# Kernel tuning notes

Hardware: AMD Instinct MI355X
Metric: run time of the kernel (lower is better)

Reference implementation:

```python
import jax, jax.numpy as jnp
import numpy as np

EMBED_DIM = 768
NUM_HEADS = 12
HEAD_DIM = EMBED_DIM // NUM_HEADS
MLP_RATIO = 4.0
HIDDEN_DIM = int(EMBED_DIM * MLP_RATIO)
B, N = 8, 1024


def setup_inputs() -> dict:
    key = jax.random.key(0)
    ks = jax.random.split(key, 12)
    d = EMBED_DIM
    h = HIDDEN_DIM
    s = lambda fan_in: 1.0 / np.sqrt(fan_in)
    return {
        "x": jax.random.normal(ks[0], (B, N, d), dtype=jnp.float32),
        "ln1_w": jnp.ones((d,), jnp.float32),
        "ln1_b": jnp.zeros((d,), jnp.float32),
        "qkv_w": jax.random.normal(ks[1], (3 * d, d), jnp.float32) * s(d),
        "qkv_b": jnp.zeros((3 * d,), jnp.float32),
        "proj_w": jax.random.normal(ks[2], (d, d), jnp.float32) * s(d),
        "proj_b": jnp.zeros((d,), jnp.float32),
        "ln2_w": jnp.ones((d,), jnp.float32),
        "ln2_b": jnp.zeros((d,), jnp.float32),
        "fc1_w": jax.random.normal(ks[3], (h, d), jnp.float32) * s(d),
        "fc1_b": jnp.zeros((h,), jnp.float32),
        "fc2_w": jax.random.normal(ks[4], (d, h), jnp.float32) * s(h),
        "fc2_b": jnp.zeros((d,), jnp.float32),
    }


def _layernorm(x, w, b, eps=1e-5):
    mu = jnp.mean(x, axis=-1, keepdims=True)
    var = jnp.var(x, axis=-1, keepdims=True)
    return (x - mu) * jax.lax.rsqrt(var + eps) * w + b


def _attention(x, qkv_w, qkv_b, proj_w, proj_b):
    b, n, c = x.shape
    qkv = x @ qkv_w.T + qkv_b  # [B, N, 3C]
    qkv = qkv.reshape(b, n, 3, NUM_HEADS, HEAD_DIM)
    q, k, v = jnp.moveaxis(qkv, 2, 0)  # each [B, N, H, Dh]
    scale = HEAD_DIM ** -0.5
    attn = jnp.einsum("bqhd,bkhd->bhqk", q, k) * scale  # [B, H, N, N]
    attn = jax.nn.softmax(attn, axis=-1)
    out = jnp.einsum("bhqk,bkhd->bqhd", attn, v).reshape(b, n, c)
    return out @ proj_w.T + proj_b


def reference(x, ln1_w, ln1_b, qkv_w, qkv_b, proj_w, proj_b,
              ln2_w, ln2_b, fc1_w, fc1_b, fc2_w, fc2_b):
    x = x + _attention(_layernorm(x, ln1_w, ln1_b), qkv_w, qkv_b, proj_w, proj_b)
    h = _layernorm(x, ln2_w, ln2_b)
    h = jax.nn.gelu(h @ fc1_w.T + fc1_b, approximate=False)
    x = x + (h @ fc2_w.T + fc2_b)
    return x
```

## Files before the change

### kernel.cpp

```cpp
#include <hip/hip_runtime.h>
#include <hip/hip_bf16.h>
#include <math.h>

typedef __attribute__((ext_vector_type(8))) short bf16x8;
typedef __attribute__((ext_vector_type(4))) float f32x4;
typedef unsigned short ushort_t;

#define GLOAD(srcp, dstp) __builtin_amdgcn_global_load_lds((const __attribute__((address_space(1))) void*)(srcp), (__attribute__((address_space(3))) void*)(dstp), 16, 0, 0)

__device__ inline ushort_t f2bfn(float f){
  union{ __bf16 h; ushort_t u; } c;
  c.h = (__bf16)f;
  return c.u;
}

__global__ __launch_bounds__(256) void cvt_all(const float* __restrict__ q, const float* __restrict__ p,
                                               const float* __restrict__ f1, const float* __restrict__ f2w,
                                               ushort_t* __restrict__ dq, ushort_t* __restrict__ dp,
                                               ushort_t* __restrict__ d1, ushort_t* __restrict__ d2){
  int i4 = blockIdx.x*256 + threadIdx.x;
  const float* src; ushort_t* dst; int off;
  if(i4 < 442368){ src=q;  dst=dq; off=i4; }
  else if(i4 < 589824){ src=p;  dst=dp; off=i4-442368; }
  else if(i4 < 1179648){ src=f1; dst=d1; off=i4-589824; }
  else { src=f2w; dst=d2; off=i4-1179648; }
  int i = off*4;
  float4 v = *(const float4*)(src+i);
  ushort4 o; o.x=f2bfn(v.x); o.y=f2bfn(v.y); o.z=f2bfn(v.z); o.w=f2bfn(v.w);
  *(ushort4*)(dst+i) = o;
}

__global__ __launch_bounds__(192) void ln_kernel(const float* __restrict__ x, const float* __restrict__ w,
                                                 const float* __restrict__ b, ushort_t* __restrict__ out){
  int row = blockIdx.x, t = threadIdx.x;
  const float4 v = *(const float4*)(x + (size_t)row*768 + t*4);
  float s  = v.x+v.y+v.z+v.w;
  float s2 = v.x*v.x+v.y*v.y+v.z*v.z+v.w*v.w;
  for(int m=1;m<64;m<<=1){ s += __shfl_xor(s,m,64); s2 += __shfl_xor(s2,m,64); }
  __shared__ float ls[3], ls2[3];
  int wv_ = t>>6;
  if((t&63)==0){ ls[wv_]=s; ls2[wv_]=s2; }
  __syncthreads();
  s = ls[0]+ls[1]+ls[2]; s2 = ls2[0]+ls2[1]+ls2[2];
  float mu = s*(1.f/768.f);
  float var = s2*(1.f/768.f) - mu*mu;
  float rs = rsqrtf(var + 1e-5f);
  float4 wv4 = *(const float4*)(w + t*4);
  float4 bv4 = *(const float4*)(b + t*4);
  ushort4 o;
  o.x = f2bfn((v.x-mu)*rs*wv4.x + bv4.x);
  o.y = f2bfn((v.y-mu)*rs*wv4.y + bv4.y);
  o.z = f2bfn((v.z-mu)*rs*wv4.z + bv4.z);
  o.w = f2bfn((v.w-mu)*rs*wv4.w + bv4.w);
  *(ushort4*)(out + (size_t)row*768 + t*4) = o;
}

template<int EPI>
__device__ __forceinline__
void gemm8_body(const ushort_t* __restrict__ A, const ushort_t* __restrict__ BT,
                const float* __restrict__ bias, void* __restrict__ out,
                int K, int Nout, int nBN)
{
  __shared__ ushort_t lds[65536];
  ushort_t* As = lds;
  ushort_t* Bs = lds + 32768;
  const int tid = threadIdx.x;
  const int lane = tid & 63, wid = tid >> 6;
  const int wm = wid >> 2, wn = wid & 3;
  const int fq = lane >> 4, fr = lane & 15;

  const int nwg = (int)gridDim.x;
  const int bid = (int)blockIdx.x;
  const int wg = (bid & 7)*(nwg>>3) + (bid>>3);
  const int bm0 = (wg / nBN) << 8;
  const int bn0 = (wg % nBN) << 8;

  const int srow0 = tid >> 2;
  const int srow1 = 128 + srow0;
  const int sgc = ((tid & 3) ^ ((srow0 >> 1) & 3)) << 3;

  auto stageA = [&](int slot, int tile, int kh){
    const int k0 = (tile<<6) + (kh<<5);
    GLOAD(A + (size_t)(bm0 + srow0)*K + k0 + sgc, As + slot*8192 + (wid*64)*8);
    GLOAD(A + (size_t)(bm0 + srow1)*K + k0 + sgc, As + slot*8192 + (512 + wid*64)*8);
  };
  auto stageB = [&](int slot, int tile, int kh){
    const int k0 = (tile<<6) + (kh<<5);
    GLOAD(BT + (size_t)(bn0 + srow0)*K + k0 + sgc, Bs + slot*8192 + (wid*64)*8);
    GLOAD(BT + (size_t)(bn0 + srow1)*K + k0 + sgc, Bs + slot*8192 + (512 + wid*64)*8);
  };

  int aoff[8], boff[4];
  #pragma unroll
  for(int m=0;m<8;m++){ int r = wm*128 + m*16 + fr; aoff[m] = r*32 + ((fq ^ ((r>>1)&3))<<3); }
  #pragma unroll
  for(int n=0;n<4;n++){ int r = wn*64  + n*16 + fr; boff[n] = r*32 + ((fq ^ ((r>>1)&3))<<3); }

  f32x4 acc[8][4];
  #pragma unroll
  for(int m=0;m<8;m++)
    #pragma unroll
    for(int n=0;n<4;n++) acc[m][n] = (f32x4){0.f,0.f,0.f,0.f};

  const int NT = K >> 6;
  stageA(0,0,0); stageB(0,0,0);
  stageA(1,0,1); stageB(1,0,1);
  stageA(2,1,0); stageB(2,1,0);
  asm volatile("s_waitcnt vmcnt(4)" ::: "memory");
  __builtin_amdgcn_s_barrier();

  for(int g=0; g<NT; ++g){
    const int par = g & 1;
    const int sl0 = par*2, sl1 = par*2 + 1;
    const int osl1 = (par^1)*2 + 1;
    bf16x8 a[8], b0, b1;

    #pragma unroll
    for(int m=0;m<8;m++) a[m] = *(const bf16x8*)(As + sl0*8192 + aoff[m]);
    b0 = *(const bf16x8*)(Bs + sl0*8192 + boff[0]);
    b1 = *(const bf16x8*)(Bs + sl0*8192 + boff[1]);
    if(g+1 < NT) stageA(osl1, g+1, 1);
    __builtin_amdgcn_s_barrier();
    asm volatile("s_waitcnt lgkmcnt(0)" ::: "memory");
    __builtin_amdgcn_s_setprio(1);
    #pragma unroll
    for(int m=0;m<8;m++){
      acc[m][0] = __builtin_amdgcn_mfma_f32_16x16x32_bf16(a[m], b0, acc[m][0], 0,0,0);
      acc[m][1] = __builtin_amdgcn_mfma_f32_16x16x32_bf16(a[m], b1, acc[m][1], 0,0,0);
    }
    __builtin_amdgcn_s_setprio(0);
    __builtin_amdgcn_s_barrier();

    b0 = *(const bf16x8*)(Bs + sl0*8192 + boff[2]);
    b1 = *(const bf16x8*)(Bs + sl0*8192 + boff[3]);
    if(g+1 < NT) stageB(osl1, g+1, 1);
    __builtin_amdgcn_s_barrier();
    asm volatile("s_waitcnt lgkmcnt(0)" ::: "memory");
    __builtin_amdgcn_s_setprio(1);
    #pragma unroll
    for(int m=0;m<8;m++){
      acc[m][2] = __builtin_amdgcn_mfma_f32_16x16x32_bf16(a[m], b0, acc[m][2], 0,0,0);
      acc[m][3] = __builtin_amdgcn_mfma_f32_16x16x32_bf16(a[m], b1, acc[m][3], 0,0,0);
    }
    __builtin_amdgcn_s_setprio(0);
    __builtin_amdgcn_s_barrier();

    #pragma unroll
    for(int m=0;m<8;m++) a[m] = *(const bf16x8*)(As + sl1*8192 + aoff[m]);
    b0 = *(const bf16x8*)(Bs + sl1*8192 + boff[0]);
    b1 = *(const bf16x8*)(Bs + sl1*8192 + boff[1]);
    if(g+2 < NT) stageA(sl0, g+2, 0);
    __builtin_amdgcn_s_barrier();
    asm volatile("s_waitcnt lgkmcnt(0)" ::: "memory");
    __builtin_amdgcn_s_setprio(1);
    #pragma unroll
    for(int m=0;m<8;m++){
      acc[m][0] = __builtin_amdgcn_mfma_f32_16x16x32_bf16(a[m], b0, acc[m][0], 0,0,0);
      acc[m][1] = __builtin_amdgcn_mfma_f32_16x16x32_bf16(a[m], b1, acc[m][1], 0,0,0);
    }
    __builtin_amdgcn_s_setprio(0);
    __builtin_amdgcn_s_barrier();

    b0 = *(const bf16x8*)(Bs + sl1*8192 + boff[2]);
    b1 = *(const bf16x8*)(Bs + sl1*8192 + boff[3]);
    if(g+2 < NT) stageB(sl0, g+2, 0);
    __builtin_amdgcn_s_barrier();
    asm volatile("s_waitcnt lgkmcnt(0)" ::: "memory");
    __builtin_amdgcn_s_setprio(1);
    #pragma unroll
    for(int m=0;m<8;m++){
      acc[m][2] = __builtin_amdgcn_mfma_f32_16x16x32_bf16(a[m], b0, acc[m][2], 0,0,0);
      acc[m][3] = __builtin_amdgcn_mfma_f32_16x16x32_bf16(a[m], b1, acc[m][3], 0,0,0);
    }
    __builtin_amdgcn_s_setprio(0);
    if(g+2 < NT){ asm volatile("s_waitcnt vmcnt(4)" ::: "memory"); }
    else        { asm volatile("s_waitcnt vmcnt(0)" ::: "memory"); }
    __builtin_amdgcn_s_barrier();
  }

  __syncthreads();
  #pragma unroll
  for(int m=0;m<8;m++){
    #pragma unroll
    for(int n=0;n<4;n++){
      int colL = wn*64 + n*16 + fr;
      float bv = bias[bn0 + colL];
      #pragma unroll
      for(int j=0;j<4;j++){
        int rowL = wm*128 + m*16 + fq*4 + j;
        float v = acc[m][n][j] + bv;
        if constexpr(EPI==2){
          float u = fminf(v*(1.0f + 0.044715f*v*v), 40.f);
          float e = exp2f(2.3020052f*u);
          v = v*e/(1.0f+e);
        }
        lds[rowL*256 + (colL ^ (((rowL>>2)&3)<<4))] = f2bfn(v);
      }
    }
  }
  __syncthreads();
  const bool isV = (EPI==0) && (bn0 >= 1536);
  if(!isV){
    #pragma unroll 4
    for(int p=0;p<16;p++){
      int flat = tid + p*512;
      int row = flat>>5;
      int c8  = flat&31;
      int col = c8*8;
      bf16x8 v8 = *(const bf16x8*)&lds[row*256 + (col ^ (((row>>2)&3)<<4))];
      int rg = bm0 + row;
      if constexpr(EPI==0){
        int colg = bn0 + col;
        int which = colg >= 768 ? 1 : 0;
        int rem = colg - which*768;
        int hh = rem>>6, dh = rem&63;
        int bb = rg>>10, np = rg&1023;
        *(bf16x8*)&((ushort_t*)out)[(((size_t)(which*96 + bb*12 + hh)*1024 + np)<<6) + dh] = v8;
      } else {
        *(bf16x8*)&((ushort_t*)out)[(size_t)rg*(size_t)Nout + bn0 + col] = v8;
      }
    }
  } else {
    #pragma unroll 4
    for(int p=0;p<16;p++){
      int flat = tid + p*512;
      int dL = flat>>5;
      int t8 = (flat&31)*8;
      ushort_t tmp[8];
      #pragma unroll
      for(int i=0;i<8;i++){
        int row = t8 + i;
        tmp[i] = lds[row*256 + (dL ^ (((row>>2)&3)<<4))];
      }
      int dg = bn0 - 1536 + dL;
      int hh = dg>>6, dh = dg&63;
      int tok0 = bm0 + t8;
      int bb = tok0>>10, np = tok0&1023;
      *(bf16x8*)&((ushort_t*)out)[((size_t)(192 + bb*12 + hh)*65536) + dh*1024 + np] = *(bf16x8*)tmp;
    }
  }
}

__global__ __launch_bounds__(512, 2)
void qkv_gemm8(const ushort_t* __restrict__ A, const ushort_t* __restrict__ BT,
               const float* __restrict__ bias, void* __restrict__ out, int K, int Nout, int nBN)
{ gemm8_body<0>(A, BT, bias, out, K, Nout, nBN); }

__global__ __launch_bounds__(512, 2)
void fc1_gemm8(const ushort_t* __restrict__ A, const ushort_t* __restrict__ BT,
               const float* __restrict__ bias, void* __restrict__ out, int K, int Nout, int nBN)
{ gemm8_body<2>(A, BT, bias, out, K, Nout, nBN); }

__device__ __forceinline__
void gemm_body_epi1(const ushort_t* __restrict__ A, const ushort_t* __restrict__ BT,
                    const float* __restrict__ bias, const float* __restrict__ resid,
                    float* __restrict__ out, int K)
{
  __shared__ ushort_t Asm[3][64*32];
  __shared__ ushort_t Bsm[3][128*32];
  const int bm0 = blockIdx.y*64;
  const int bn0 = blockIdx.x*128;
  const int tid = threadIdx.x;
  const int lane = tid & 63;
  const int wid = tid >> 6;
  const int wn = wid;
  const int fq = lane>>4, fr = lane&15;

  const int rA = tid>>2, cA = (tid&3)*8;
  const int e0 = (wid*2)*512 + lane*8;
  const int e1 = (wid*2+1)*512 + lane*8;
  const int r0 = e0>>5, c0 = e0&31;
  const int r1 = e1>>5, c1 = e1&31;

  f32x4 acc[4][2];
  for(int m=0;m<4;m++) for(int n=0;n<2;n++) acc[m][n] = (f32x4){0.f,0.f,0.f,0.f};

  auto STAGE = [&](int buf, int k0){
    GLOAD(A  + (size_t)(bm0+rA)*K + k0 + cA, &Asm[buf][wid*512]);
    GLOAD(BT + (size_t)(bn0+r0)*K + k0 + c0, &Bsm[buf][(wid*2)*512]);
    GLOAD(BT + (size_t)(bn0+r1)*K + k0 + c1, &Bsm[buf][(wid*2+1)*512]);
  };

  const int NT = K>>5;
  STAGE(0, 0);
  STAGE(1, 32);
  asm volatile("s_waitcnt vmcnt(3)" ::: "memory");
  __builtin_amdgcn_s_barrier();

  int cur = 0;
  for(int kt=0; kt<NT; ++kt){
    if(kt+2 < NT){
      int sbuf = cur+2; if(sbuf>=3) sbuf-=3;
      STAGE(sbuf, (kt+2)<<5);
    }
    bf16x8 af[4], bfr[2];
    for(int m=0;m<4;m++)
      af[m] = *(const bf16x8*)(&Asm[cur][(m*16 + fr)*32 + fq*8]);
    for(int n=0;n<2;n++)
      bfr[n] = *(const bf16x8*)(&Bsm[cur][(wn*32 + n*16 + fr)*32 + fq*8]);
    for(int m=0;m<4;m++)
      for(int n=0;n<2;n++)
        acc[m][n] = __builtin_amdgcn_mfma_f32_16x16x32_bf16(af[m], bfr[n], acc[m][n], 0,0,0);
    if(kt+1 < NT){
      if(kt+2 < NT){ asm volatile("s_waitcnt vmcnt(3)" ::: "memory"); }
      else         { asm volatile("s_waitcnt vmcnt(0)" ::: "memory"); }
      __builtin_amdgcn_s_barrier();
    }
    cur++; if(cur>=3) cur-=3;
  }

  for(int m=0;m<4;m++){
    int row0 = bm0 + m*16 + fq*4;
    for(int n=0;n<2;n++){
      int col = bn0 + wn*32 + n*16 + fr;
      float bv = bias[col];
      for(int j=0;j<4;j++){
        int r = row0 + j;
        float v = acc[m][n][j] + bv + resid[(size_t)r*768 + col];
        out[(size_t)r*768 + col] = v;
      }
    }
  }
}

__global__ __launch_bounds__(256)
void proj_gemm(const ushort_t* __restrict__ A, const ushort_t* __restrict__ BT,
               const float* __restrict__ bias, const float* __restrict__ resid,
               float* __restrict__ out, int K)
{ gemm_body_epi1(A, BT, bias, resid, out, K); }

__global__ __launch_bounds__(256)
void fc2_gemm(const ushort_t* __restrict__ A, const ushort_t* __restrict__ BT,
              const float* __restrict__ bias, const float* __restrict__ resid,
              float* __restrict__ out, int K)
{ gemm_body_epi1(A, BT, bias, resid, out, K); }

__global__ __launch_bounds__(256)
void attn_kernel(const ushort_t* __restrict__ qkv, ushort_t* __restrict__ outp)
{
  __shared__ ushort_t Ksm[2][64*72];
  __shared__ ushort_t Vt[2][64*72];
  __shared__ ushort_t Psm[4][16*72];
  const int bh = blockIdx.y;
  const int q0 = blockIdx.x*64;
  const int tid = threadIdx.x, lane = tid&63, wid = tid>>6;
  const int fq = lane>>4, fr = lane&15;
  const ushort_t* Qb = qkv + ((size_t)bh*1024)*64;
  const ushort_t* Kb = qkv + ((size_t)(96 + bh)*1024)*64;
  const ushort_t* Vb = qkv + ((size_t)(192 + bh))*65536;

  bf16x8 ones;
  #pragma unroll
  for(int i=0;i<8;i++) ones[i] = (short)0x3F80;

  bf16x8 qf[2];
  {
    int qr = q0 + wid*16 + fr;
    qf[0] = *(const bf16x8*)(Qb + (size_t)qr*64 +      fq*8);
    qf[1] = *(const bf16x8*)(Qb + (size_t)qr*64 + 32 + fq*8);
  }
  f32x4 o[4];
  for(int dt=0;dt<4;dt++) o[dt] = (f32x4){0.f,0.f,0.f,0.f};
  float lrun[4];
  for(int j=0;j<4;j++) lrun[j]=0.f;

  const float c1 = 0.18033688f;

  const int sr = tid>>3, sc = (tid&7)*8;

  bf16x8 k0r = *(const bf16x8*)(Kb + (size_t)sr*64 + sc);
  bf16x8 k1r = *(const bf16x8*)(Kb + (size_t)(sr+32)*64 + sc);
  bf16x8 v0r = *(const bf16x8*)(Vb + (size_t)sr*1024 + sc);
  bf16x8 v1r = *(const bf16x8*)(Vb + (size_t)(sr+32)*1024 + sc);
  *(bf16x8*)(Ksm[0] + sr*72 + sc)      = k0r;
  *(bf16x8*)(Ksm[0] + (sr+32)*72 + sc) = k1r;
  *(bf16x8*)(Vt[0]  + sr*72 + sc)      = v0r;
  *(bf16x8*)(Vt[0]  + (sr+32)*72 + sc) = v1r;

  int cur = 0;
  for(int kt=0; kt<16; kt++){
    __syncthreads();
    if(kt+1 < 16){
      int kv1 = (kt+1)*64;
      k0r = *(const bf16x8*)(Kb + (size_t)(kv1+sr)*64 + sc);
      k1r = *(const bf16x8*)(Kb + (size_t)(kv1+sr+32)*64 + sc);
      v0r = *(const bf16x8*)(Vb + (size_t)sr*1024 + kv1 + sc);
      v1r = *(const bf16x8*)(Vb + (size_t)(sr+32)*1024 + kv1 + sc);
    }

    f32x4 s[4];
    for(int ct=0;ct<4;ct++){
      bf16x8 kf0 = *(const bf16x8*)(Ksm[cur] + (ct*16 + fr)*72 +      fq*8);
      bf16x8 kf1 = *(const bf16x8*)(Ksm[cur] + (ct*16 + fr)*72 + 32 + fq*8);
      f32x4 z = (f32x4){0.f,0.f,0.f,0.f};
      z = __builtin_amdgcn_mfma_f32_16x16x32_bf16(qf[0], kf0, z, 0,0,0);
      z = __builtin_amdgcn_mfma_f32_16x16x32_bf16(qf[1], kf1, z, 0,0,0);
      s[ct] = z;
    }

    #pragma unroll
    for(int ct=0;ct<4;ct++){
      #pragma unroll
      for(int j=0;j<4;j++){
        float p = exp2f(s[ct][j]*c1);
        int g = (ct*2 + (fr>>3)) ^ fq;
        Psm[wid][(fq*4 + j)*72 + g*8 + (fr&7)] = f2bfn(p);
      }
    }

    bf16x8 pf[2];
    {
      int key = (fr>>2)&3;
      pf[0] = *(const bf16x8*)(&Psm[wid][fr*72 + ((0*4+fq)^key)*8]);
      pf[1] = *(const bf16x8*)(&Psm[wid][fr*72 + ((1*4+fq)^key)*8]);
    }
    f32x4 o5 = (f32x4){0.f,0.f,0.f,0.f};
    o5 = __builtin_amdgcn_mfma_f32_16x16x32_bf16(pf[0], ones, o5, 0,0,0);
    o5 = __builtin_amdgcn_mfma_f32_16x16x32_bf16(pf[1], ones, o5, 0,0,0);
    #pragma unroll
    for(int j=0;j<4;j++) lrun[j] += o5[j];

    for(int dt=0;dt<4;dt++){
      for(int kc=0;kc<2;kc++){
        bf16x8 vf = *(const bf16x8*)(Vt[cur] + (dt*16 + fr)*72 + kc*32 + fq*8);
        o[dt] = __builtin_amdgcn_mfma_f32_16x16x32_bf16(pf[kc], vf, o[dt], 0,0,0);
      }
    }

    if(kt+1 < 16){
      *(bf16x8*)(Ksm[cur^1] + sr*72 + sc)      = k0r;
      *(bf16x8*)(Ksm[cur^1] + (sr+32)*72 + sc) = k1r;
      *(bf16x8*)(Vt[cur^1]  + sr*72 + sc)      = v0r;
      *(bf16x8*)(Vt[cur^1]  + (sr+32)*72 + sc) = v1r;
    }
    cur ^= 1;
  }

  int b = bh/12, h = bh%12;
  for(int dt=0;dt<4;dt++){
    for(int j=0;j<4;j++){
      int qr = q0 + wid*16 + fq*4 + j;
      float v = o[dt][j] / lrun[j];
      outp[(size_t)(b*1024 + qr)*768 + h*64 + dt*16 + fr] = f2bfn(v);
    }
  }
}

extern "C" void kernel_launch(void* const* d_in, const int* in_sizes, int n_in,
                              void* d_out, int out_size, void* d_ws, size_t ws_size,
                              hipStream_t stream)
{
  const float* x     = (const float*)d_in[0];
  const float* ln1w  = (const float*)d_in[1];
  const float* ln1b  = (const float*)d_in[2];
  const float* qkvw  = (const float*)d_in[3];
  const float* qkvb  = (const float*)d_in[4];
  const float* projw = (const float*)d_in[5];
  const float* projb = (const float*)d_in[6];
  const float* ln2w  = (const float*)d_in[7];
  const float* ln2b  = (const float*)d_in[8];
  const float* fc1w  = (const float*)d_in[9];
  const float* fc1b  = (const float*)d_in[10];
  const float* fc2w  = (const float*)d_in[11];
  const float* fc2b  = (const float*)d_in[12];

  char* ws = (char*)d_ws;
  size_t off = 0;
  auto alloc = [&](size_t bytes){ char* p = ws + off; off += (bytes + 255) & ~255ULL; return p; };
  ushort_t* wq = (ushort_t*)alloc((size_t)2304*768*2);
  ushort_t* wp = (ushort_t*)alloc((size_t)768*768*2);
  ushort_t* w1 = (ushort_t*)alloc((size_t)3072*768*2);
  ushort_t* w2 = (ushort_t*)alloc((size_t)768*3072*2);
  ushort_t* lnbuf  = (ushort_t*)alloc((size_t)8192*768*2);
  ushort_t* qkvbuf = (ushort_t*)alloc((size_t)3*96*1024*64*2);
  ushort_t* attno  = (ushort_t*)alloc((size_t)8192*768*2);
  ushort_t* hbuf   = qkvbuf;
  float* x1 = (float*)d_out;

  cvt_all<<<6912, 256, 0, stream>>>(qkvw, projw, fc1w, fc2w, wq, wp, w1, w2);
  ln_kernel<<<8192, 192, 0, stream>>>(x, ln1w, ln1b, lnbuf);
  qkv_gemm8<<<288, 512, 0, stream>>>(lnbuf, wq, qkvb, qkvbuf, 768, 2304, 9);
  attn_kernel<<<dim3(16,96), 256, 0, stream>>>(qkvbuf, attno);
  proj_gemm<<<dim3(6,128), 256, 0, stream>>>(attno, wp, projb, x, x1, 768);
  ln_kernel<<<8192, 192, 0, stream>>>(x1, ln2w, ln2b, lnbuf);
  fc1_gemm8<<<384, 512, 0, stream>>>(lnbuf, w1, fc1b, hbuf, 768, 3072, 12);
  fc2_gemm<<<dim3(6,128), 256, 0, stream>>>(hbuf, w2, fc2b, x1, (float*)d_out, 3072);
}
```

Before: 325.1 us.

## Swizzle LDS, deepen pipeline to 4 stages, remap blocks across XCDs in proj/fc2 GEMMs

The proj and fc2 GEMM kernels now use a 1D grid whose block ids are remapped so that consecutive tiles land on the same XCD, aiming for better L2 reuse. LDS tiles are XOR-swizzled to cut bank conflicts on the bf16x8 fragment reads. Prefetch depth goes from 3 to 4 buffers, with the vmcnt waits adjusted. This costs more LDS per block, which may lower occupancy.

```diff
diff --git a/kernel.cpp b/kernel.cpp
--- a/kernel.cpp
+++ b/kernel.cpp
@@ -254,59 +254,71 @@
 __device__ __forceinline__
 void gemm_body_epi1(const ushort_t* __restrict__ A, const ushort_t* __restrict__ BT,
                     const float* __restrict__ bias, const float* __restrict__ resid,
-                    float* __restrict__ out, int K)
+                    float* __restrict__ out, int K, int nBN)
 {
-  __shared__ ushort_t Asm[3][64*32];
-  __shared__ ushort_t Bsm[3][128*32];
-  const int bm0 = blockIdx.y*64;
-  const int bn0 = blockIdx.x*128;
+  __shared__ ushort_t Asm[4][64*32];
+  __shared__ ushort_t Bsm[4][128*32];
+  const int nwg = (int)gridDim.x;
+  const int bid = (int)blockIdx.x;
+  const int wg = (bid & 7)*(nwg>>3) + (bid>>3);
+  const int bm0 = (wg / nBN) * 64;
+  const int bn0 = (wg % nBN) * 128;
   const int tid = threadIdx.x;
   const int lane = tid & 63;
   const int wid = tid >> 6;
   const int wn = wid;
   const int fq = lane>>4, fr = lane&15;
 
-  const int rA = tid>>2, cA = (tid&3)*8;
-  const int e0 = (wid*2)*512 + lane*8;
-  const int e1 = (wid*2+1)*512 + lane*8;
-  const int r0 = e0>>5, c0 = e0&31;
-  const int r1 = e1>>5, c1 = e1&31;
+  const int rA = tid>>2;
+  const int cAs = ((tid&3) ^ ((rA>>1)&3))<<3;
+  const int r0 = wid*32 + (lane>>2);
+  const int r1 = r0 + 16;
+  const int cBs = ((lane&3) ^ ((r0>>1)&3))<<3;
 
   f32x4 acc[4][2];
   for(int m=0;m<4;m++) for(int n=0;n<2;n++) acc[m][n] = (f32x4){0.f,0.f,0.f,0.f};
 
   auto STAGE = [&](int buf, int k0){
-    GLOAD(A  + (size_t)(bm0+rA)*K + k0 + cA, &Asm[buf][wid*512]);
-    GLOAD(BT + (size_t)(bn0+r0)*K + k0 + c0, &Bsm[buf][(wid*2)*512]);
-    GLOAD(BT + (size_t)(bn0+r1)*K + k0 + c1, &Bsm[buf][(wid*2+1)*512]);
+    GLOAD(A  + (size_t)(bm0+rA)*K + k0 + cAs, &Asm[buf][wid*512]);
+    GLOAD(BT + (size_t)(bn0+r0)*K + k0 + cBs, &Bsm[buf][(wid*2)*512]);
+    GLOAD(BT + (size_t)(bn0+r1)*K + k0 + cBs, &Bsm[buf][(wid*2+1)*512]);
   };
+
+  int aoff[4], boff[2];
+  #pragma unroll
+  for(int m=0;m<4;m++){ int r = m*16 + fr; aoff[m] = r*32 + ((fq ^ ((r>>1)&3))<<3); }
+  #pragma unroll
+  for(int n=0;n<2;n++){ int r = wn*32 + n*16 + fr; boff[n] = r*32 + ((fq ^ ((r>>1)&3))<<3); }
 
   const int NT = K>>5;
   STAGE(0, 0);
   STAGE(1, 32);
-  asm volatile("s_waitcnt vmcnt(3)" ::: "memory");
+  STAGE(2, 64);
+  asm volatile("s_waitcnt vmcnt(6)" ::: "memory");
   __builtin_amdgcn_s_barrier();
 
   int cur = 0;
   for(int kt=0; kt<NT; ++kt){
-    if(kt+2 < NT){
-      int sbuf = cur+2; if(sbuf>=3) sbuf-=3;
-      STAGE(sbuf, (kt+2)<<5);
-    }
+    if(kt+3 < NT) STAGE((cur+3)&3, (kt+3)<<5);
     bf16x8 af[4], bfr[2];
+    #pragma unroll
     for(int m=0;m<4;m++)
-      af[m] = *(const bf16x8*)(&Asm[cur][(m*16 + fr)*32 + fq*8]);
+      af[m] = *(const bf16x8*)(&Asm[cur][aoff[m]]);
+    #pragma unroll
     for(int n=0;n<2;n++)
-      bfr[n] = *(const bf16x8*)(&Bsm[cur][(wn*32 + n*16 + fr)*32 + fq*8]);
+      bfr[n] = *(const bf16x8*)(&Bsm[cur][boff[n]]);
+    #pragma unroll
     for(int m=0;m<4;m++)
+      #pragma unroll
       for(int n=0;n<2;n++)
         acc[m][n] = __builtin_amdgcn_mfma_f32_16x16x32_bf16(af[m], bfr[n], acc[m][n], 0,0,0);
     if(kt+1 < NT){
-      if(kt+2 < NT){ asm volatile("s_waitcnt vmcnt(3)" ::: "memory"); }
-      else         { asm volatile("s_waitcnt vmcnt(0)" ::: "memory"); }
+      if(kt+3 < NT)      { asm volatile("s_waitcnt vmcnt(6)" ::: "memory"); }
+      else if(kt+2 < NT) { asm volatile("s_waitcnt vmcnt(3)" ::: "memory"); }
+      else               { asm volatile("s_waitcnt vmcnt(0)" ::: "memory"); }
       __builtin_amdgcn_s_barrier();
     }
-    cur++; if(cur>=3) cur-=3;
+    cur = (cur+1)&3;
   }
 
   for(int m=0;m<4;m++){
@@ -326,14 +338,14 @@
 __global__ __launch_bounds__(256)
 void proj_gemm(const ushort_t* __restrict__ A, const ushort_t* __restrict__ BT,
                const float* __restrict__ bias, const float* __restrict__ resid,
-               float* __restrict__ out, int K)
-{ gemm_body_epi1(A, BT, bias, resid, out, K); }
+               float* __restrict__ out, int K, int nBN)
+{ gemm_body_epi1(A, BT, bias, resid, out, K, nBN); }
 
 __global__ __launch_bounds__(256)
 void fc2_gemm(const ushort_t* __restrict__ A, const ushort_t* __restrict__ BT,
               const float* __restrict__ bias, const float* __restrict__ resid,
-              float* __restrict__ out, int K)
-{ gemm_body_epi1(A, BT, bias, resid, out, K); }
+              float* __restrict__ out, int K, int nBN)
+{ gemm_body_epi1(A, BT, bias, resid, out, K, nBN); }
 
 __global__ __launch_bounds__(256)
 void attn_kernel(const ushort_t* __restrict__ qkv, ushort_t* __restrict__ outp)
@@ -481,8 +493,8 @@
   ln_kernel<<<8192, 192, 0, stream>>>(x, ln1w, ln1b, lnbuf);
   qkv_gemm8<<<288, 512, 0, stream>>>(lnbuf, wq, qkvb, qkvbuf, 768, 2304, 9);
   attn_kernel<<<dim3(16,96), 256, 0, stream>>>(qkvbuf, attno);
-  proj_gemm<<<dim3(6,128), 256, 0, stream>>>(attno, wp, projb, x, x1, 768);
+  proj_gemm<<<768, 256, 0, stream>>>(attno, wp, projb, x, x1, 768, 6);
   ln_kernel<<<8192, 192, 0, stream>>>(x1, ln2w, ln2b, lnbuf);
   fc1_gemm8<<<384, 512, 0, stream>>>(lnbuf, w1, fc1b, hbuf, 768, 3072, 12);
-  fc2_gemm<<<dim3(6,128), 256, 0, stream>>>(hbuf, w2, fc2b, x1, (float*)d_out, 3072);
-}
+  fc2_gemm<<<768, 256, 0, stream>>>(hbuf, w2, fc2b, x1, (float*)d_out, 3072, 6);
+}
```

New measurement: 313.9 us. -3.5%, faster.
